# Kernel optimization log

Hardware: AMD Instinct MI355X
Metric: run time of the kernel (lower is better)

Reference implementation:

```python
import jax, jax.numpy as jnp
import numpy as np

B, N, T, D = 256, 64, 60, 128
H = 128  # gate hidden dims


def setup_inputs() -> dict:
    key = jax.random.key(0)
    ks = jax.random.split(key, 5)
    x = jax.random.normal(ks[0], (B, N, T, D), dtype=jnp.float32)
    s = 1.0 / np.sqrt(D)
    sg_w1 = jax.random.normal(ks[1], (D, H), dtype=jnp.float32) * s
    sg_b1 = jnp.zeros((H,), dtype=jnp.float32)
    sg_w2 = jax.random.normal(ks[2], (H, 1), dtype=jnp.float32) * (1.0 / np.sqrt(H))
    sg_b2 = jnp.zeros((1,), dtype=jnp.float32)
    tg_w1 = jax.random.normal(ks[3], (D, H), dtype=jnp.float32) * s
    tg_b1 = jnp.zeros((H,), dtype=jnp.float32)
    tg_w2 = jax.random.normal(ks[4], (H, 1), dtype=jnp.float32) * (1.0 / np.sqrt(H))
    tg_b2 = jnp.zeros((1,), dtype=jnp.float32)
    return {"x": x, "sg_w1": sg_w1, "sg_b1": sg_b1, "sg_w2": sg_w2, "sg_b2": sg_b2,
            "tg_w1": tg_w1, "tg_b1": tg_b1, "tg_w2": tg_w2, "tg_b2": tg_b2}


def reference(x, sg_w1, sg_b1, sg_w2, sg_b2, tg_w1, tg_b1, tg_w2, tg_b2):
    # Spatial attentional aggregation, vectorized over all timesteps at once.
    # Segment softmax over batch_index == softmax over the node axis (regular segments).
    gate = jnp.tanh(x @ sg_w1 + sg_b1) @ sg_w2 + sg_b2          # [B, N, T, 1]
    alpha = jax.nn.softmax(gate, axis=1)                        # softmax over nodes
    pooled = jnp.sum(alpha * x, axis=1)                         # [B, T, D]
    # Temporal attention pooling over the sequence axis.
    score = jnp.tanh(pooled @ tg_w1 + tg_b1) @ tg_w2 + tg_b2    # [B, T, 1]
    tw = jax.nn.softmax(score, axis=1)                          # [B, T, 1]
    final = jnp.sum(tw * pooled, axis=1)                        # [B, D]
    return final, tw
```

## Files before the change

kernel.cpp:

```cpp
#include <hip/hip_runtime.h>

#define B_ 256
#define N_ 64
#define T_ 60
#define D_ 128
#define H_ 128

typedef __attribute__((ext_vector_type(8))) short short8;
typedef __attribute__((ext_vector_type(4))) float f32x4;

__device__ __forceinline__ unsigned short f2bf(float f) {
  unsigned int u = __builtin_bit_cast(unsigned int, f);
  u = u + 0x7FFFu + ((u >> 16) & 1u);
  return (unsigned short)(u >> 16);
}

__device__ __forceinline__ float tanh_fast(float x) {
  float e = __builtin_amdgcn_exp2f(x * 2.885390081777927f);
  return 1.0f - 2.0f * __builtin_amdgcn_rcpf(e + 1.0f);
}

__global__ __launch_bounds__(256) void prep_weights(
    const float* __restrict__ sg_w1, const float* __restrict__ tg_w1,
    unsigned short* __restrict__ wfrag) {
  int tid = blockIdx.x * 256 + threadIdx.x;
  if (tid >= 2 * 4 * 8 * 64) return;
  int l  = tid & 63;
  int nt = (tid >> 6) & 7;
  int kt = (tid >> 9) & 3;
  int m  = tid >> 11;
  const float* W = m ? tg_w1 : sg_w1;
  int n  = nt * 16 + (l & 15);
  int k0 = kt * 32 + 8 * (l >> 4);
  unsigned short* dst = wfrag + (size_t)tid * 8;
#pragma unroll
  for (int i = 0; i < 8; ++i) dst[i] = f2bf(W[(k0 + i) * H_ + n]);
}

__global__ __launch_bounds__(256) void spatial_kernel(
    const float* __restrict__ x,
    const short8* __restrict__ wfrag,
    const float* __restrict__ b1,
    const float* __restrict__ w2,
    const float* __restrict__ b2p,
    float* __restrict__ pooled) {
  __shared__ float xs[64][132];
  __shared__ float gate_lds[64];
  __shared__ float alpha_lds[64];
  __shared__ float pp[2][128];

  const int tid = threadIdx.x;
  const int bid = blockIdx.x;
  const int b = bid / T_;
  const int t = bid - b * T_;

  const float* xbase = x + ((size_t)b * N_ * T_ + t) * D_;
#pragma unroll
  for (int it = 0; it < 8; ++it) {
    int q = it * 256 + tid;
    int n = q >> 5;
    int c4 = (q & 31) << 2;
    float4 v = *(const float4*)(xbase + (size_t)n * (T_ * D_) + c4);
    *(float4*)(&xs[n][c4]) = v;
  }
  __syncthreads();

  const int l = tid & 63;
  const int w = tid >> 6;
  const int lg = l >> 4;
  const int lr = l & 15;

  float b1v[8], w2v[8];
#pragma unroll
  for (int nt = 0; nt < 8; ++nt) {
    b1v[nt] = b1[nt * 16 + lr];
    w2v[nt] = w2[nt * 16 + lr];
  }
  const float b2 = b2p[0];

  f32x4 acc[8];
#pragma unroll
  for (int nt = 0; nt < 8; ++nt) acc[nt] = (f32x4)(0.0f);

  const int row = 16 * w + lr;
#pragma unroll
  for (int kt = 0; kt < 4; ++kt) {
    const int k0 = kt * 32 + 8 * lg;
    float4 a0 = *(const float4*)(&xs[row][k0]);
    float4 a1 = *(const float4*)(&xs[row][k0 + 4]);
    short8 af;
    af[0] = (short)f2bf(a0.x); af[1] = (short)f2bf(a0.y);
    af[2] = (short)f2bf(a0.z); af[3] = (short)f2bf(a0.w);
    af[4] = (short)f2bf(a1.x); af[5] = (short)f2bf(a1.y);
    af[6] = (short)f2bf(a1.z); af[7] = (short)f2bf(a1.w);
#pragma unroll
    for (int nt = 0; nt < 8; ++nt) {
      short8 bf = wfrag[(kt * 8 + nt) * 64 + l];
      acc[nt] = __builtin_amdgcn_mfma_f32_16x16x32_bf16(af, bf, acc[nt], 0, 0, 0);
    }
  }

#pragma unroll
  for (int j = 0; j < 4; ++j) {
    float s = 0.f;
#pragma unroll
    for (int nt = 0; nt < 8; ++nt) {
      float h = acc[nt][j] + b1v[nt];
      s += tanh_fast(h) * w2v[nt];
    }
    s += __shfl_xor(s, 1);
    s += __shfl_xor(s, 2);
    s += __shfl_xor(s, 4);
    s += __shfl_xor(s, 8);
    if (lr == 0) gate_lds[16 * w + 4 * lg + j] = s + b2;
  }
  __syncthreads();

  float g = gate_lds[l];
  float mx = g;
  mx = fmaxf(mx, __shfl_xor(mx, 32));
  mx = fmaxf(mx, __shfl_xor(mx, 16));
  mx = fmaxf(mx, __shfl_xor(mx, 8));
  mx = fmaxf(mx, __shfl_xor(mx, 4));
  mx = fmaxf(mx, __shfl_xor(mx, 2));
  mx = fmaxf(mx, __shfl_xor(mx, 1));
  float p = __builtin_amdgcn_exp2f((g - mx) * 1.4426950408889634f);
  float sm = p;
  sm += __shfl_xor(sm, 32);
  sm += __shfl_xor(sm, 16);
  sm += __shfl_xor(sm, 8);
  sm += __shfl_xor(sm, 4);
  sm += __shfl_xor(sm, 2);
  sm += __shfl_xor(sm, 1);
  float alpha = p / sm;
  if (w == 0) alpha_lds[l] = alpha;
  __syncthreads();

  const int c = tid & 127;
  const int hh = tid >> 7;
  float s = 0.f;
#pragma unroll
  for (int i = 0; i < 32; ++i) {
    int n = 32 * hh + i;
    s += alpha_lds[n] * xs[n][c];
  }
  pp[hh][c] = s;
  __syncthreads();
  if (tid < 128) {
    pooled[((size_t)b * T_ + t) * D_ + tid] = pp[0][tid] + pp[1][tid];
  }
}

__global__ __launch_bounds__(256) void temporal_kernel(
    const float* __restrict__ pooled,
    const short8* __restrict__ wfrag,
    const float* __restrict__ b1,
    const float* __restrict__ w2,
    const float* __restrict__ b2p,
    float* __restrict__ out) {
  __shared__ float xs[64][132];
  __shared__ float score_lds[64];
  __shared__ float tw_lds[64];
  __shared__ float pp[2][128];

  const int tid = threadIdx.x;
  const int b = blockIdx.x;

  const float* pb = pooled + (size_t)b * T_ * D_;
#pragma unroll
  for (int it = 0; it < 8; ++it) {
    int q = it * 256 + tid;
    int n = q >> 5;
    int c4 = (q & 31) << 2;
    float4 v = {0.f, 0.f, 0.f, 0.f};
    if (n < T_) v = *(const float4*)(pb + n * D_ + c4);
    *(float4*)(&xs[n][c4]) = v;
  }
  __syncthreads();

  const int l = tid & 63;
  const int w = tid >> 6;
  const int lg = l >> 4;
  const int lr = l & 15;

  float b1v[8], w2v[8];
#pragma unroll
  for (int nt = 0; nt < 8; ++nt) {
    b1v[nt] = b1[nt * 16 + lr];
    w2v[nt] = w2[nt * 16 + lr];
  }
  const float b2 = b2p[0];

  f32x4 acc[8];
#pragma unroll
  for (int nt = 0; nt < 8; ++nt) acc[nt] = (f32x4)(0.0f);

  const int row = 16 * w + lr;
#pragma unroll
  for (int kt = 0; kt < 4; ++kt) {
    const int k0 = kt * 32 + 8 * lg;
    float4 a0 = *(const float4*)(&xs[row][k0]);
    float4 a1 = *(const float4*)(&xs[row][k0 + 4]);
    short8 af;
    af[0] = (short)f2bf(a0.x); af[1] = (short)f2bf(a0.y);
    af[2] = (short)f2bf(a0.z); af[3] = (short)f2bf(a0.w);
    af[4] = (short)f2bf(a1.x); af[5] = (short)f2bf(a1.y);
    af[6] = (short)f2bf(a1.z); af[7] = (short)f2bf(a1.w);
#pragma unroll
    for (int nt = 0; nt < 8; ++nt) {
      short8 bf = wfrag[(kt * 8 + nt) * 64 + l];
      acc[nt] = __builtin_amdgcn_mfma_f32_16x16x32_bf16(af, bf, acc[nt], 0, 0, 0);
    }
  }

#pragma unroll
  for (int j = 0; j < 4; ++j) {
    float s = 0.f;
#pragma unroll
    for (int nt = 0; nt < 8; ++nt) {
      float h = acc[nt][j] + b1v[nt];
      s += tanh_fast(h) * w2v[nt];
    }
    s += __shfl_xor(s, 1);
    s += __shfl_xor(s, 2);
    s += __shfl_xor(s, 4);
    s += __shfl_xor(s, 8);
    if (lr == 0) score_lds[16 * w + 4 * lg + j] = s + b2;
  }
  __syncthreads();

  float g = (l < T_) ? score_lds[l] : -3.0e38f;
  float mx = g;
  mx = fmaxf(mx, __shfl_xor(mx, 32));
  mx = fmaxf(mx, __shfl_xor(mx, 16));
  mx = fmaxf(mx, __shfl_xor(mx, 8));
  mx = fmaxf(mx, __shfl_xor(mx, 4));
  mx = fmaxf(mx, __shfl_xor(mx, 2));
  mx = fmaxf(mx, __shfl_xor(mx, 1));
  float p = (l < T_) ? __builtin_amdgcn_exp2f((g - mx) * 1.4426950408889634f) : 0.f;
  float sm = p;
  sm += __shfl_xor(sm, 32);
  sm += __shfl_xor(sm, 16);
  sm += __shfl_xor(sm, 8);
  sm += __shfl_xor(sm, 4);
  sm += __shfl_xor(sm, 2);
  sm += __shfl_xor(sm, 1);
  float tw = p / sm;
  if (w == 0) {
    tw_lds[l] = tw;
    if (l < T_) out[B_ * D_ + b * T_ + l] = tw;
  }
  __syncthreads();

  const int c = tid & 127;
  const int hh = tid >> 7;
  float s = 0.f;
#pragma unroll
  for (int i = 0; i < 30; ++i) {
    int tt = 30 * hh + i;
    s += tw_lds[tt] * xs[tt][c];
  }
  pp[hh][c] = s;
  __syncthreads();
  if (tid < 128) out[(size_t)b * D_ + tid] = pp[0][tid] + pp[1][tid];
}

extern "C" void kernel_launch(void* const* d_in, const int* in_sizes, int n_in,
                              void* d_out, int out_size, void* d_ws, size_t ws_size,
                              hipStream_t stream) {
  const float* x     = (const float*)d_in[0];
  const float* sg_w1 = (const float*)d_in[1];
  const float* sg_b1 = (const float*)d_in[2];
  const float* sg_w2 = (const float*)d_in[3];
  const float* sg_b2 = (const float*)d_in[4];
  const float* tg_w1 = (const float*)d_in[5];
  const float* tg_b1 = (const float*)d_in[6];
  const float* tg_w2 = (const float*)d_in[7];
  const float* tg_b2 = (const float*)d_in[8];
  float* out = (float*)d_out;

  unsigned short* wfrag = (unsigned short*)d_ws;
  float* pooled = (float*)((char*)d_ws + 65536);

  prep_weights<<<16, 256, 0, stream>>>(sg_w1, tg_w1, wfrag);
  spatial_kernel<<<B_ * T_, 256, 0, stream>>>(
      x, (const short8*)wfrag, sg_b1, sg_w2, sg_b2, pooled);
  temporal_kernel<<<B_, 256, 0, stream>>>(
      pooled, (const short8*)(wfrag + 16384), tg_b1, tg_w2, tg_b2, out);
}
```

Measured before the change: 149.1 us.

## Make spatial kernel persistent over timesteps with register prefetch of next x tile

```diff
diff --git a/kernel.cpp b/kernel.cpp
--- a/kernel.cpp
+++ b/kernel.cpp
@@ -5,6 +5,7 @@
 #define T_ 60
 #define D_ 128
 #define H_ 128
+#define TPB 30
 
 typedef __attribute__((ext_vector_type(8))) short short8;
 typedef __attribute__((ext_vector_type(4))) float f32x4;
@@ -18,6 +19,12 @@
 __device__ __forceinline__ float tanh_fast(float x) {
   float e = __builtin_amdgcn_exp2f(x * 2.885390081777927f);
   return 1.0f - 2.0f * __builtin_amdgcn_rcpf(e + 1.0f);
+}
+
+__device__ __forceinline__ void lds_barrier() {
+  asm volatile("s_waitcnt lgkmcnt(0)" ::: "memory");
+  __builtin_amdgcn_s_barrier();
+  asm volatile("" ::: "memory");
 }
 
 __global__ __launch_bounds__(256) void prep_weights(
@@ -37,30 +44,186 @@
   for (int i = 0; i < 8; ++i) dst[i] = f2bf(W[(k0 + i) * H_ + n]);
 }
 
-__global__ __launch_bounds__(256) void spatial_kernel(
+__global__ __launch_bounds__(256, 2) void spatial_kernel(
     const float* __restrict__ x,
     const short8* __restrict__ wfrag,
     const float* __restrict__ b1,
     const float* __restrict__ w2,
-    const float* __restrict__ b2p,
     float* __restrict__ pooled) {
   __shared__ float xs[64][132];
-  __shared__ float gate_lds[64];
+  __shared__ float gpart[2][64];
   __shared__ float alpha_lds[64];
-  __shared__ float pp[2][128];
+  __shared__ f32x4 pp[8][32];
 
   const int tid = threadIdx.x;
   const int bid = blockIdx.x;
-  const int b = bid / T_;
-  const int t = bid - b * T_;
-
-  const float* xbase = x + ((size_t)b * N_ * T_ + t) * D_;
+  const int b  = bid >> 1;
+  const int t0 = (bid & 1) * TPB;
+  const float* xb = x + (size_t)b * (N_ * T_ * D_);
+
+  const int l  = tid & 63;
+  const int w  = tid >> 6;
+  const int lg = l >> 4;
+  const int lr = l & 15;
+  const int wr = w >> 1;
+  const int wc = w & 1;
+
+  short8 wfb[4][4];
+#pragma unroll
+  for (int kt = 0; kt < 4; ++kt)
+#pragma unroll
+    for (int ntl = 0; ntl < 4; ++ntl)
+      wfb[kt][ntl] = wfrag[(kt * 8 + wc * 4 + ntl) * 64 + l];
+
+  float b1v[4], w2v[4];
+#pragma unroll
+  for (int ntl = 0; ntl < 4; ++ntl) {
+    b1v[ntl] = b1[wc * 64 + ntl * 16 + lr];
+    w2v[ntl] = w2[wc * 64 + ntl * 16 + lr];
+  }
+
+  float4 px[8];
+#pragma unroll
+  for (int it = 0; it < 8; ++it) {
+    int q = it * 256 + tid; int n = q >> 5; int c4 = (q & 31) << 2;
+    px[it] = *(const float4*)(xb + (size_t)n * (T_ * D_) + (size_t)t0 * D_ + c4);
+  }
+#pragma unroll
+  for (int it = 0; it < 8; ++it) {
+    int q = it * 256 + tid; int n = q >> 5; int c4 = (q & 31) << 2;
+    *(float4*)&xs[n][c4] = px[it];
+  }
+  lds_barrier();
+
+  for (int ti = 0; ti < TPB; ++ti) {
+    const int t = t0 + ti;
+
+    if (ti + 1 < TPB) {
+#pragma unroll
+      for (int it = 0; it < 8; ++it) {
+        int q = it * 256 + tid; int n = q >> 5; int c4 = (q & 31) << 2;
+        px[it] = *(const float4*)(xb + (size_t)n * (T_ * D_) + (size_t)(t + 1) * D_ + c4);
+      }
+    }
+
+    f32x4 acc[2][4];
+#pragma unroll
+    for (int mt = 0; mt < 2; ++mt)
+#pragma unroll
+      for (int ntl = 0; ntl < 4; ++ntl) acc[mt][ntl] = (f32x4)(0.0f);
+
+#pragma unroll
+    for (int kt = 0; kt < 4; ++kt) {
+      const int k0 = kt * 32 + 8 * lg;
+#pragma unroll
+      for (int mt = 0; mt < 2; ++mt) {
+        const int row = wr * 32 + mt * 16 + lr;
+        float4 a0 = *(const float4*)&xs[row][k0];
+        float4 a1 = *(const float4*)&xs[row][k0 + 4];
+        short8 af;
+        af[0] = (short)f2bf(a0.x); af[1] = (short)f2bf(a0.y);
+        af[2] = (short)f2bf(a0.z); af[3] = (short)f2bf(a0.w);
+        af[4] = (short)f2bf(a1.x); af[5] = (short)f2bf(a1.y);
+        af[6] = (short)f2bf(a1.z); af[7] = (short)f2bf(a1.w);
+#pragma unroll
+        for (int ntl = 0; ntl < 4; ++ntl)
+          acc[mt][ntl] = __builtin_amdgcn_mfma_f32_16x16x32_bf16(af, wfb[kt][ntl], acc[mt][ntl], 0, 0, 0);
+      }
+    }
+
+#pragma unroll
+    for (int mt = 0; mt < 2; ++mt) {
+#pragma unroll
+      for (int j = 0; j < 4; ++j) {
+        float s = 0.f;
+#pragma unroll
+        for (int ntl = 0; ntl < 4; ++ntl) {
+          float h = acc[mt][ntl][j] + b1v[ntl];
+          s += tanh_fast(h) * w2v[ntl];
+        }
+        s += __shfl_xor(s, 1);
+        s += __shfl_xor(s, 2);
+        s += __shfl_xor(s, 4);
+        s += __shfl_xor(s, 8);
+        if (lr == 0) gpart[wc][wr * 32 + mt * 16 + 4 * lg + j] = s;
+      }
+    }
+    lds_barrier();
+
+    {
+      float g = gpart[0][l] + gpart[1][l];
+      float mx = g;
+      mx = fmaxf(mx, __shfl_xor(mx, 32));
+      mx = fmaxf(mx, __shfl_xor(mx, 16));
+      mx = fmaxf(mx, __shfl_xor(mx, 8));
+      mx = fmaxf(mx, __shfl_xor(mx, 4));
+      mx = fmaxf(mx, __shfl_xor(mx, 2));
+      mx = fmaxf(mx, __shfl_xor(mx, 1));
+      float p = __builtin_amdgcn_exp2f((g - mx) * 1.4426950408889634f);
+      float sm = p;
+      sm += __shfl_xor(sm, 32);
+      sm += __shfl_xor(sm, 16);
+      sm += __shfl_xor(sm, 8);
+      sm += __shfl_xor(sm, 4);
+      sm += __shfl_xor(sm, 2);
+      sm += __shfl_xor(sm, 1);
+      if (w == 0) alpha_lds[l] = p / sm;
+    }
+    lds_barrier();
+
+    {
+      const int hh = tid >> 5, cg = tid & 31;
+      f32x4 s4 = (f32x4)(0.0f);
+#pragma unroll
+      for (int i = 0; i < 8; ++i) {
+        int n = hh * 8 + i;
+        f32x4 v = *(const f32x4*)&xs[n][cg * 4];
+        s4 += alpha_lds[n] * v;
+      }
+      pp[hh][cg] = s4;
+    }
+    lds_barrier();
+
+    if (ti + 1 < TPB) {
+#pragma unroll
+      for (int it = 0; it < 8; ++it) {
+        int q = it * 256 + tid; int n = q >> 5; int c4 = (q & 31) << 2;
+        *(float4*)&xs[n][c4] = px[it];
+      }
+    }
+    if (tid < 128) {
+      const float* ppf = (const float*)pp;
+      float s = 0.f;
+#pragma unroll
+      for (int h2 = 0; h2 < 8; ++h2) s += ppf[h2 * 128 + tid];
+      pooled[((size_t)b * T_ + t) * D_ + tid] = s;
+    }
+    lds_barrier();
+  }
+}
+
+__global__ __launch_bounds__(256) void temporal_kernel(
+    const float* __restrict__ pooled,
+    const short8* __restrict__ wfrag,
+    const float* __restrict__ b1,
+    const float* __restrict__ w2,
+    float* __restrict__ out) {
+  __shared__ float xs[64][132];
+  __shared__ float score_lds[64];
+  __shared__ float tw_lds[64];
+  __shared__ float pp[2][128];
+
+  const int tid = threadIdx.x;
+  const int b = blockIdx.x;
+
+  const float* pb = pooled + (size_t)b * T_ * D_;
 #pragma unroll
   for (int it = 0; it < 8; ++it) {
     int q = it * 256 + tid;
     int n = q >> 5;
     int c4 = (q & 31) << 2;
-    float4 v = *(const float4*)(xbase + (size_t)n * (T_ * D_) + c4);
+    float4 v = {0.f, 0.f, 0.f, 0.f};
+    if (n < T_) v = *(const float4*)(pb + n * D_ + c4);
     *(float4*)(&xs[n][c4]) = v;
   }
   __syncthreads();
@@ -76,7 +239,6 @@
     b1v[nt] = b1[nt * 16 + lr];
     w2v[nt] = w2[nt * 16 + lr];
   }
-  const float b2 = b2p[0];
 
   f32x4 acc[8];
 #pragma unroll
@@ -112,120 +274,7 @@
     s += __shfl_xor(s, 2);
     s += __shfl_xor(s, 4);
     s += __shfl_xor(s, 8);
-    if (lr == 0) gate_lds[16 * w + 4 * lg + j] = s + b2;
-  }
-  __syncthreads();
-
-  float g = gate_lds[l];
-  float mx = g;
-  mx = fmaxf(mx, __shfl_xor(mx, 32));
-  mx = fmaxf(mx, __shfl_xor(mx, 16));
-  mx = fmaxf(mx, __shfl_xor(mx, 8));
-  mx = fmaxf(mx, __shfl_xor(mx, 4));
-  mx = fmaxf(mx, __shfl_xor(mx, 2));
-  mx = fmaxf(mx, __shfl_xor(mx, 1));
-  float p = __builtin_amdgcn_exp2f((g - mx) * 1.4426950408889634f);
-  float sm = p;
-  sm += __shfl_xor(sm, 32);
-  sm += __shfl_xor(sm, 16);
-  sm += __shfl_xor(sm, 8);
-  sm += __shfl_xor(sm, 4);
-  sm += __shfl_xor(sm, 2);
-  sm += __shfl_xor(sm, 1);
-  float alpha = p / sm;
-  if (w == 0) alpha_lds[l] = alpha;
-  __syncthreads();
-
-  const int c = tid & 127;
-  const int hh = tid >> 7;
-  float s = 0.f;
-#pragma unroll
-  for (int i = 0; i < 32; ++i) {
-    int n = 32 * hh + i;
-    s += alpha_lds[n] * xs[n][c];
-  }
-  pp[hh][c] = s;
-  __syncthreads();
-  if (tid < 128) {
-    pooled[((size_t)b * T_ + t) * D_ + tid] = pp[0][tid] + pp[1][tid];
-  }
-}
-
-__global__ __launch_bounds__(256) void temporal_kernel(
-    const float* __restrict__ pooled,
-    const short8* __restrict__ wfrag,
-    const float* __restrict__ b1,
-    const float* __restrict__ w2,
-    const float* __restrict__ b2p,
-    float* __restrict__ out) {
-  __shared__ float xs[64][132];
-  __shared__ float score_lds[64];
-  __shared__ float tw_lds[64];
-  __shared__ float pp[2][128];
-
-  const int tid = threadIdx.x;
-  const int b = blockIdx.x;
-
-  const float* pb = pooled + (size_t)b * T_ * D_;
-#pragma unroll
-  for (int it = 0; it < 8; ++it) {
-    int q = it * 256 + tid;
-    int n = q >> 5;
-    int c4 = (q & 31) << 2;
-    float4 v = {0.f, 0.f, 0.f, 0.f};
-    if (n < T_) v = *(const float4*)(pb + n * D_ + c4);
-    *(float4*)(&xs[n][c4]) = v;
-  }
-  __syncthreads();
-
-  const int l = tid & 63;
-  const int w = tid >> 6;
-  const int lg = l >> 4;
-  const int lr = l & 15;
-
-  float b1v[8], w2v[8];
-#pragma unroll
-  for (int nt = 0; nt < 8; ++nt) {
-    b1v[nt] = b1[nt * 16 + lr];
-    w2v[nt] = w2[nt * 16 + lr];
-  }
-  const float b2 = b2p[0];
-
-  f32x4 acc[8];
-#pragma unroll
-  for (int nt = 0; nt < 8; ++nt) acc[nt] = (f32x4)(0.0f);
-
-  const int row = 16 * w + lr;
-#pragma unroll
-  for (int kt = 0; kt < 4; ++kt) {
-    const int k0 = kt * 32 + 8 * lg;
-    float4 a0 = *(const float4*)(&xs[row][k0]);
-    float4 a1 = *(const float4*)(&xs[row][k0 + 4]);
-    short8 af;
-    af[0] = (short)f2bf(a0.x); af[1] = (short)f2bf(a0.y);
-    af[2] = (short)f2bf(a0.z); af[3] = (short)f2bf(a0.w);
-    af[4] = (short)f2bf(a1.x); af[5] = (short)f2bf(a1.y);
-    af[6] = (short)f2bf(a1.z); af[7] = (short)f2bf(a1.w);
-#pragma unroll
-    for (int nt = 0; nt < 8; ++nt) {
-      short8 bf = wfrag[(kt * 8 + nt) * 64 + l];
-      acc[nt] = __builtin_amdgcn_mfma_f32_16x16x32_bf16(af, bf, acc[nt], 0, 0, 0);
-    }
-  }
-
-#pragma unroll
-  for (int j = 0; j < 4; ++j) {
-    float s = 0.f;
-#pragma unroll
-    for (int nt = 0; nt < 8; ++nt) {
-      float h = acc[nt][j] + b1v[nt];
-      s += tanh_fast(h) * w2v[nt];
-    }
-    s += __shfl_xor(s, 1);
-    s += __shfl_xor(s, 2);
-    s += __shfl_xor(s, 4);
-    s += __shfl_xor(s, 8);
-    if (lr == 0) score_lds[16 * w + 4 * lg + j] = s + b2;
+    if (lr == 0) score_lds[16 * w + 4 * lg + j] = s;
   }
   __syncthreads();
 
@@ -272,19 +321,17 @@
   const float* sg_w1 = (const float*)d_in[1];
   const float* sg_b1 = (const float*)d_in[2];
   const float* sg_w2 = (const float*)d_in[3];
-  const float* sg_b2 = (const float*)d_in[4];
   const float* tg_w1 = (const float*)d_in[5];
   const float* tg_b1 = (const float*)d_in[6];
   const float* tg_w2 = (const float*)d_in[7];
-  const float* tg_b2 = (const float*)d_in[8];
   float* out = (float*)d_out;
 
   unsigned short* wfrag = (unsigned short*)d_ws;
   float* pooled = (float*)((char*)d_ws + 65536);
 
   prep_weights<<<16, 256, 0, stream>>>(sg_w1, tg_w1, wfrag);
-  spatial_kernel<<<B_ * T_, 256, 0, stream>>>(
-      x, (const short8*)wfrag, sg_b1, sg_w2, sg_b2, pooled);
+  spatial_kernel<<<B_ * (T_ / TPB), 256, 0, stream>>>(
+      x, (const short8*)wfrag, sg_b1, sg_w2, pooled);
   temporal_kernel<<<B_, 256, 0, stream>>>(
-      pooled, (const short8*)(wfrag + 16384), tg_b1, tg_w2, tg_b2, out);
-}
+      pooled, (const short8*)(wfrag + 16384), tg_b1, tg_w2, out);
+}
```

Result: slower. 363.3 us (+143.7%).

## Stage x as bf16 in LDS, re-read x from cache for pooling, drop softmax max

Applied to the files above, without the earlier changes.

```diff
diff --git a/kernel.cpp b/kernel.cpp
--- a/kernel.cpp
+++ b/kernel.cpp
@@ -37,30 +37,131 @@
   for (int i = 0; i < 8; ++i) dst[i] = f2bf(W[(k0 + i) * H_ + n]);
 }
 
-__global__ __launch_bounds__(256) void spatial_kernel(
+__global__ __launch_bounds__(256, 4) void spatial_kernel(
     const float* __restrict__ x,
     const short8* __restrict__ wfrag,
     const float* __restrict__ b1,
     const float* __restrict__ w2,
-    const float* __restrict__ b2p,
     float* __restrict__ pooled) {
-  __shared__ float xs[64][132];
-  __shared__ float gate_lds[64];
-  __shared__ float alpha_lds[64];
-  __shared__ float pp[2][128];
+  __shared__ __align__(16) char xs16[64 * 272];
+  __shared__ float gpart[64];
 
   const int tid = threadIdx.x;
   const int bid = blockIdx.x;
   const int b = bid / T_;
   const int t = bid - b * T_;
 
-  const float* xbase = x + ((size_t)b * N_ * T_ + t) * D_;
+  const float* xb = x + (size_t)b * (N_ * T_ * D_) + (size_t)t * D_;
+
+  const int cg  = tid >> 3;
+  const int sub = tid & 7;
+  const int l   = tid & 63;
+  const int w   = tid >> 6;
+  const int lg  = l >> 4;
+  const int lr  = l & 15;
+
+#pragma unroll
+  for (int r = 0; r < 8; ++r) {
+    const int n = sub + 8 * r;
+    float4 v = *(const float4*)(xb + (size_t)n * (T_ * D_) + 4 * cg);
+    unsigned lo = ((unsigned)f2bf(v.y) << 16) | f2bf(v.x);
+    unsigned hi = ((unsigned)f2bf(v.w) << 16) | f2bf(v.z);
+    *(uint2*)(xs16 + n * 272 + cg * 8) = make_uint2(lo, hi);
+  }
+  __syncthreads();
+
+  float b1v[8], w2v[8];
+#pragma unroll
+  for (int nt = 0; nt < 8; ++nt) {
+    b1v[nt] = b1[nt * 16 + lr];
+    w2v[nt] = w2[nt * 16 + lr];
+  }
+
+  f32x4 acc[8];
+#pragma unroll
+  for (int nt = 0; nt < 8; ++nt) acc[nt] = (f32x4)(0.0f);
+
+  const int row = 16 * w + lr;
+  const char* abase = xs16 + row * 272 + lg * 16;
+#pragma unroll
+  for (int kt = 0; kt < 4; ++kt) {
+    short8 af = *(const short8*)(abase + kt * 64);
+#pragma unroll
+    for (int nt = 0; nt < 8; ++nt) {
+      short8 bf = wfrag[(kt * 8 + nt) * 64 + l];
+      acc[nt] = __builtin_amdgcn_mfma_f32_16x16x32_bf16(af, bf, acc[nt], 0, 0, 0);
+    }
+  }
+
+#pragma unroll
+  for (int j = 0; j < 4; ++j) {
+    float s = 0.f;
+#pragma unroll
+    for (int nt = 0; nt < 8; ++nt) {
+      float h = acc[nt][j] + b1v[nt];
+      s += tanh_fast(h) * w2v[nt];
+    }
+    s += __shfl_xor(s, 1);
+    s += __shfl_xor(s, 2);
+    s += __shfl_xor(s, 4);
+    s += __shfl_xor(s, 8);
+    if (lr == 0) gpart[16 * w + 4 * lg + j] = s;
+  }
+  __syncthreads();
+
+  float p = __builtin_amdgcn_exp2f(gpart[l] * 1.4426950408889634f);
+  float sm = p;
+  sm += __shfl_xor(sm, 32);
+  sm += __shfl_xor(sm, 16);
+  sm += __shfl_xor(sm, 8);
+  sm += __shfl_xor(sm, 4);
+  sm += __shfl_xor(sm, 2);
+  sm += __shfl_xor(sm, 1);
+  const float alpha = p * __builtin_amdgcn_rcpf(sm);
+
+  const float* xb2 = xb;
+  asm volatile("" : "+r"(xb2));
+  f32x4 q = (f32x4)(0.0f);
+#pragma unroll
+  for (int r = 0; r < 8; ++r) {
+    const int n = sub + 8 * r;
+    const float av = __shfl(alpha, n);
+    f32x4 v = *(const f32x4*)(xb2 + (size_t)n * (T_ * D_) + 4 * cg);
+    q += av * v;
+  }
+#pragma unroll
+  for (int m = 1; m <= 4; m <<= 1) {
+    q[0] += __shfl_xor(q[0], m);
+    q[1] += __shfl_xor(q[1], m);
+    q[2] += __shfl_xor(q[2], m);
+    q[3] += __shfl_xor(q[3], m);
+  }
+  if (sub == 0)
+    *(f32x4*)(pooled + ((size_t)b * T_ + t) * D_ + 4 * cg) = q;
+}
+
+__global__ __launch_bounds__(256) void temporal_kernel(
+    const float* __restrict__ pooled,
+    const short8* __restrict__ wfrag,
+    const float* __restrict__ b1,
+    const float* __restrict__ w2,
+    float* __restrict__ out) {
+  __shared__ float xs[64][132];
+  __shared__ float score_lds[64];
+  __shared__ float tw_lds[64];
+  __shared__ float pp[2][128];
+
+  const int tid = threadIdx.x;
+  const int b = blockIdx.x;
+
+  const float* pb = pooled + (size_t)b * T_ * D_;
 #pragma unroll
   for (int it = 0; it < 8; ++it) {
     int q = it * 256 + tid;
     int n = q >> 5;
     int c4 = (q & 31) << 2;
-    float4 v = *(const float4*)(xbase + (size_t)n * (T_ * D_) + c4);
+    float4 v = {0.f, 0.f, 0.f, 0.f};
+    if (n < T_) v = *(const float4*)(pb + n * D_ + c4);
     *(float4*)(&xs[n][c4]) = v;
   }
   __syncthreads();
@@ -76,7 +177,6 @@
     b1v[nt] = b1[nt * 16 + lr];
     w2v[nt] = w2[nt * 16 + lr];
   }
-  const float b2 = b2p[0];
 
   f32x4 acc[8];
 #pragma unroll
@@ -112,132 +212,11 @@
     s += __shfl_xor(s, 2);
     s += __shfl_xor(s, 4);
     s += __shfl_xor(s, 8);
-    if (lr == 0) gate_lds[16 * w + 4 * lg + j] = s + b2;
-  }
-  __syncthreads();
-
-  float g = gate_lds[l];
-  float mx = g;
-  mx = fmaxf(mx, __shfl_xor(mx, 32));
-  mx = fmaxf(mx, __shfl_xor(mx, 16));
-  mx = fmaxf(mx, __shfl_xor(mx, 8));
-  mx = fmaxf(mx, __shfl_xor(mx, 4));
-  mx = fmaxf(mx, __shfl_xor(mx, 2));
-  mx = fmaxf(mx, __shfl_xor(mx, 1));
-  float p = __builtin_amdgcn_exp2f((g - mx) * 1.4426950408889634f);
-  float sm = p;
-  sm += __shfl_xor(sm, 32);
-  sm += __shfl_xor(sm, 16);
-  sm += __shfl_xor(sm, 8);
-  sm += __shfl_xor(sm, 4);
-  sm += __shfl_xor(sm, 2);
-  sm += __shfl_xor(sm, 1);
-  float alpha = p / sm;
-  if (w == 0) alpha_lds[l] = alpha;
-  __syncthreads();
-
-  const int c = tid & 127;
-  const int hh = tid >> 7;
-  float s = 0.f;
-#pragma unroll
-  for (int i = 0; i < 32; ++i) {
-    int n = 32 * hh + i;
-    s += alpha_lds[n] * xs[n][c];
-  }
-  pp[hh][c] = s;
-  __syncthreads();
-  if (tid < 128) {
-    pooled[((size_t)b * T_ + t) * D_ + tid] = pp[0][tid] + pp[1][tid];
-  }
-}
-
-__global__ __launch_bounds__(256) void temporal_kernel(
-    const float* __restrict__ pooled,
-    const short8* __restrict__ wfrag,
-    const float* __restrict__ b1,
-    const float* __restrict__ w2,
-    const float* __restrict__ b2p,
-    float* __restrict__ out) {
-  __shared__ float xs[64][132];
-  __shared__ float score_lds[64];
-  __shared__ float tw_lds[64];
-  __shared__ float pp[2][128];
-
-  const int tid = threadIdx.x;
-  const int b = blockIdx.x;
-
-  const float* pb = pooled + (size_t)b * T_ * D_;
-#pragma unroll
-  for (int it = 0; it < 8; ++it) {
-    int q = it * 256 + tid;
-    int n = q >> 5;
-    int c4 = (q & 31) << 2;
-    float4 v = {0.f, 0.f, 0.f, 0.f};
-    if (n < T_) v = *(const float4*)(pb + n * D_ + c4);
-    *(float4*)(&xs[n][c4]) = v;
-  }
-  __syncthreads();
-
-  const int l = tid & 63;
-  const int w = tid >> 6;
-  const int lg = l >> 4;
-  const int lr = l & 15;
-
-  float b1v[8], w2v[8];
-#pragma unroll
-  for (int nt = 0; nt < 8; ++nt) {
-    b1v[nt] = b1[nt * 16 + lr];
-    w2v[nt] = w2[nt * 16 + lr];
-  }
-  const float b2 = b2p[0];
-
-  f32x4 acc[8];
-#pragma unroll
-  for (int nt = 0; nt < 8; ++nt) acc[nt] = (f32x4)(0.0f);
-
-  const int row = 16 * w + lr;
-#pragma unroll
-  for (int kt = 0; kt < 4; ++kt) {
-    const int k0 = kt * 32 + 8 * lg;
-    float4 a0 = *(const float4*)(&xs[row][k0]);
-    float4 a1 = *(const float4*)(&xs[row][k0 + 4]);
-    short8 af;
-    af[0] = (short)f2bf(a0.x); af[1] = (short)f2bf(a0.y);
-    af[2] = (short)f2bf(a0.z); af[3] = (short)f2bf(a0.w);
-    af[4] = (short)f2bf(a1.x); af[5] = (short)f2bf(a1.y);
-    af[6] = (short)f2bf(a1.z); af[7] = (short)f2bf(a1.w);
-#pragma unroll
-    for (int nt = 0; nt < 8; ++nt) {
-      short8 bf = wfrag[(kt * 8 + nt) * 64 + l];
-      acc[nt] = __builtin_amdgcn_mfma_f32_16x16x32_bf16(af, bf, acc[nt], 0, 0, 0);
-    }
-  }
-
-#pragma unroll
-  for (int j = 0; j < 4; ++j) {
-    float s = 0.f;
-#pragma unroll
-    for (int nt = 0; nt < 8; ++nt) {
-      float h = acc[nt][j] + b1v[nt];
-      s += tanh_fast(h) * w2v[nt];
-    }
-    s += __shfl_xor(s, 1);
-    s += __shfl_xor(s, 2);
-    s += __shfl_xor(s, 4);
-    s += __shfl_xor(s, 8);
-    if (lr == 0) score_lds[16 * w + 4 * lg + j] = s + b2;
-  }
-  __syncthreads();
-
-  float g = (l < T_) ? score_lds[l] : -3.0e38f;
-  float mx = g;
-  mx = fmaxf(mx, __shfl_xor(mx, 32));
-  mx = fmaxf(mx, __shfl_xor(mx, 16));
-  mx = fmaxf(mx, __shfl_xor(mx, 8));
-  mx = fmaxf(mx, __shfl_xor(mx, 4));
-  mx = fmaxf(mx, __shfl_xor(mx, 2));
-  mx = fmaxf(mx, __shfl_xor(mx, 1));
-  float p = (l < T_) ? __builtin_amdgcn_exp2f((g - mx) * 1.4426950408889634f) : 0.f;
+    if (lr == 0) score_lds[16 * w + 4 * lg + j] = s;
+  }
+  __syncthreads();
+
+  float p = (l < T_) ? __builtin_amdgcn_exp2f(score_lds[l] * 1.4426950408889634f) : 0.f;
   float sm = p;
   sm += __shfl_xor(sm, 32);
   sm += __shfl_xor(sm, 16);
@@ -272,11 +251,9 @@
   const float* sg_w1 = (const float*)d_in[1];
   const float* sg_b1 = (const float*)d_in[2];
   const float* sg_w2 = (const float*)d_in[3];
-  const float* sg_b2 = (const float*)d_in[4];
   const float* tg_w1 = (const float*)d_in[5];
   const float* tg_b1 = (const float*)d_in[6];
   const float* tg_w2 = (const float*)d_in[7];
-  const float* tg_b2 = (const float*)d_in[8];
   float* out = (float*)d_out;
 
   unsigned short* wfrag = (unsigned short*)d_ws;
@@ -284,7 +261,7 @@
 
   prep_weights<<<16, 256, 0, stream>>>(sg_w1, tg_w1, wfrag);
   spatial_kernel<<<B_ * T_, 256, 0, stream>>>(
-      x, (const short8*)wfrag, sg_b1, sg_w2, sg_b2, pooled);
+      x, (const short8*)wfrag, sg_b1, sg_w2, pooled);
   temporal_kernel<<<B_, 256, 0, stream>>>(
-      pooled, (const short8*)(wfrag + 16384), tg_b1, tg_w2, tg_b2, out);
-}
+      pooled, (const short8*)(wfrag + 16384), tg_b1, tg_w2, out);
+}
```

Measured after the change: 211.7 us. 1.42x slower.
